# Performance work log

Measured on AMD Instinct MI355X. Metric: run time of the kernel, lower is better.

The kernel has to match this reference:

```python
import jax, jax.numpy as jnp
import numpy as np

N, E, D, H1, H2 = 50000, 800000, 128, 128, 128


def setup_inputs() -> dict:
    key = jax.random.key(0)
    ks = jax.random.split(key, 9)
    s = 0.05
    return {
        "x": jax.random.normal(ks[0], (N, D), dtype=jnp.float32),
        "edge_index": jax.random.randint(ks[1], (2, E), 0, N, dtype=jnp.int64),
        "W_l1": jax.random.normal(ks[2], (D, H1), dtype=jnp.float32) * s,
        "b_l1": jnp.zeros((H1,), dtype=jnp.float32),
        "W_r1": jax.random.normal(ks[3], (D, H1), dtype=jnp.float32) * s,
        "W_l2": jax.random.normal(ks[4], (H1, H2), dtype=jnp.float32) * s,
        "b_l2": jnp.zeros((H2,), dtype=jnp.float32),
        "W_r2": jax.random.normal(ks[5], (H1, H2), dtype=jnp.float32) * s,
        "W_e": jax.random.normal(ks[6], (2 * H2, 1), dtype=jnp.float32) * s,
        "b_e": jnp.zeros((1,), dtype=jnp.float32),
    }


def _sage_conv(h, src, tgt, n_nodes, W_l, b_l, W_r):
    # PyG SAGEConv (mean aggr): out = lin_l(mean_{j in N(i)} h_j) + lin_r(h_i)
    msg = h[src]                                              # [E, F] gather
    agg = jax.ops.segment_sum(msg, tgt, num_segments=n_nodes)  # [N, F]
    cnt = jax.ops.segment_sum(jnp.ones((src.shape[0], 1), h.dtype), tgt,
                              num_segments=n_nodes)            # [N, 1]
    mean = agg / jnp.maximum(cnt, 1.0)                         # empty nbrs -> 0
    return mean @ W_l + b_l + h @ W_r


def reference(x, edge_index, W_l1, b_l1, W_r1, W_l2, b_l2, W_r2, W_e, b_e):
    src, tgt = edge_index[0], edge_index[1]
    n_nodes = x.shape[0]
    h = jax.nn.relu(_sage_conv(x, src, tgt, n_nodes, W_l1, b_l1, W_r1))
    # dropout is identity in eval mode
    h = _sage_conv(h, src, tgt, n_nodes, W_l2, b_l2, W_r2)
    z = jnp.concatenate([h[src], h[tgt]], axis=-1)  # [E, 2*H2]
    y = z @ W_e + b_e                                # [E, 1]
    return jax.nn.sigmoid(y)
```

## Files before the change

kernel.cpp:

```cpp
#include <hip/hip_runtime.h>

#define NN 50000
#define NE 800000
#define DD 128
#define BUCKETS 196
#define PB 4096
#define PBLK 196
#define EMAX 6144
#define BPAD 264
#define PACKB 3125
#define WTB 128

typedef unsigned int uint_t;
typedef unsigned short ush_t;
typedef __attribute__((ext_vector_type(8))) short short8;
typedef __attribute__((ext_vector_type(4))) float f32x4;

__device__ __forceinline__ float bflo(uint_t u) { return __uint_as_float(u << 16); }
__device__ __forceinline__ float bfhi(uint_t u) { return __uint_as_float(u & 0xffff0000u); }
__device__ __forceinline__ ush_t f2bf(float f) {
  uint_t u = __float_as_uint(f);
  u += 0x7fffu + ((u >> 16) & 1u);
  return (ush_t)(u >> 16);
}
__device__ __forceinline__ uint_t pack2(float a, float b) {
  return (uint_t)f2bf(a) | ((uint_t)f2bf(b) << 16);
}

__device__ __forceinline__ int ld_idx(const void* ei, int is64, long long i) {
  return is64 ? (int)((const long long*)ei)[i] : ((const int*)ei)[i];
}

__device__ __forceinline__ int detect64(const void* ei) {
  const unsigned long long* p = (const unsigned long long*)ei;
  unsigned long long w = p[threadIdx.x & 63];
  return __ballot((w >> 32) != 0) == 0ull ? 1 : 0;
}

__device__ __forceinline__ int block_incl_scan(int v, int tid, int* wsum) {
  int lane = tid & 63, wave = tid >> 6;
  int s = v;
#pragma unroll
  for (int off = 1; off < 64; off <<= 1) {
    int u = __shfl_up(s, off, 64);
    if (lane >= off) s += u;
  }
  if (lane == 63) wsum[wave] = s;
  __syncthreads();
  int base = 0;
  if (wave > 0) base += wsum[0];
  if (wave > 1) base += wsum[1];
  if (wave > 2) base += wsum[2];
  return base + s;
}

__global__ __launch_bounds__(256) void prep_part_k(
    const void* __restrict__ ei, int* __restrict__ bcur,
    uint_t* __restrict__ pbuf, uint_t* __restrict__ epk,
    const float* __restrict__ x, ush_t* __restrict__ xbc,
    const float* __restrict__ Wl1, const float* __restrict__ Wr1,
    const float* __restrict__ Wl2, const float* __restrict__ Wr2,
    const float* __restrict__ We, const float* __restrict__ bl2,
    const float* __restrict__ be,
    ush_t* __restrict__ Wt1, float* __restrict__ uv, float* __restrict__ cc) {
  __shared__ int hist[256];
  __shared__ int basel[256];
  __shared__ int cur[256];
  __shared__ int gbase[256];
  __shared__ int wsum[4];
  __shared__ uint_t buf[PB];
  __shared__ unsigned char bbuf[PB];
  int tid = threadIdx.x;
  int blk = blockIdx.x;
  if (blk >= PBLK) {
    int blk2 = blk - PBLK;
    if (blk2 < 2) {
      const float* W = blk2 ? Wr2 : Wl2;
      int base = blk2 * 256;
      int wave = tid >> 6, lane = tid & 63;
      float e0 = We[lane], e1 = We[64 + lane];
      float f0 = We[128 + lane], f1 = We[192 + lane];
      for (int k = wave * 32; k < wave * 32 + 32; ++k) {
        float m0 = W[k * DD + lane];
        float m1 = W[k * DD + 64 + lane];
        float p = m0 * e0 + m1 * e1;
        float q = m0 * f0 + m1 * f1;
#pragma unroll
        for (int off = 32; off > 0; off >>= 1) {
          p += __shfl_down(p, off, 64);
          q += __shfl_down(q, off, 64);
        }
        if (lane == 0) {
          uv[base + k] = p;
          uv[base + 128 + k] = q;
        }
      }
      return;
    }
    if (blk2 == 2) {
      if (tid < 64) {
        int k = tid;
        float p = bl2[k] * (We[k] + We[128 + k]) +
                  bl2[k + 64] * (We[k + 64] + We[192 + k]);
#pragma unroll
        for (int off = 32; off > 0; off >>= 1) p += __shfl_down(p, off, 64);
        if (k == 0) cc[0] = p + be[0];
      }
      return;
    }
    blk2 -= 3;
    if (blk2 < PACKB) {
      int i = blk2 * 256 + tid;
      int node = i >> 4;
      int g = i & 15;
      const float4* xp = reinterpret_cast<const float4*>(x) + (size_t)i * 2;
      float4 v0 = xp[0];
      float4 v1 = xp[1];
      uint4 o;
      o.x = pack2(v0.x, v0.y);
      o.y = pack2(v0.z, v0.w);
      o.z = pack2(v1.x, v1.y);
      o.w = pack2(v1.z, v1.w);
      int chunk = g >> 2;
      int off32 = (g & 3) * 8;
      *reinterpret_cast<uint4*>(xbc + ((size_t)chunk * NN + node) * 32 + off32) = o;
      return;
    }
    blk2 -= PACKB;
    int e = blk2 * 256 + tid;
    int col = e >> 8;
    int k = e & 255;
    float v = (k < DD) ? Wl1[k * DD + col] : Wr1[(k - DD) * DD + col];
    Wt1[col * 256 + k] = f2bf(v);
    return;
  }
  int is64 = detect64(ei);
  hist[tid] = 0;
  __syncthreads();
  long long base = (long long)blk * PB;
  uint_t pv[PB / 256];
#pragma unroll
  for (int i = 0; i < PB / 256; ++i) {
    long long e = base + i * 256 + tid;
    if (e < NE) {
      int s = ld_idx(ei, is64, e);
      int d = ld_idx(ei, is64, (long long)NE + e);
      pv[i] = ((uint_t)(d >> 8) << 24) | ((uint_t)(d & 255) << 16) | (uint_t)s;
      epk[e] = ((uint_t)d << 16) | (uint_t)s;
      atomicAdd(&hist[d >> 8], 1);
    } else {
      pv[i] = 0xFFFFFFFFu;
    }
  }
  __syncthreads();
  int hv = hist[tid];
  int incl = block_incl_scan(hv, tid, wsum);
  basel[tid] = incl - hv;
  cur[tid] = incl - hv;
  if (hv > 0) gbase[tid] = atomicAdd(&bcur[tid], hv);
  __syncthreads();
#pragma unroll
  for (int i = 0; i < PB / 256; ++i) {
    uint_t p = pv[i];
    if (p != 0xFFFFFFFFu) {
      int b = p >> 24;
      int r = atomicAdd(&cur[b], 1);
      buf[r] = p & 0xFFFFFFu;
      bbuf[r] = (unsigned char)b;
    }
  }
  __syncthreads();
  int total = basel[255] + hist[255];
  for (int j = tid; j < total; j += 256) {
    int b = bbuf[j];
    int slot = gbase[b] + (j - basel[b]);
    if (slot < EMAX) pbuf[(size_t)b * EMAX + slot] = buf[j];
  }
}

__global__ __launch_bounds__(256) void csr_k(const uint_t* __restrict__ pbuf,
                                             const int* __restrict__ bcur,
                                             int* __restrict__ offsets,
                                             ush_t* __restrict__ srclist) {
  __shared__ int cnt[256];
  __shared__ int scur[256];
  __shared__ int wsum[4];
  __shared__ int sgb, scnt, stot;
  __shared__ uint_t ebuf[EMAX];
  int tid = threadIdx.x;
  int b = blockIdx.x;
  int v = 0;
  if (tid < BUCKETS) {
    v = bcur[tid];
    if (v > EMAX) v = EMAX;
  }
  int incl = block_incl_scan(v, tid, wsum);
  if (tid == b) { sgb = incl - v; scnt = v; }
  if (tid == BUCKETS - 1) stot = incl;
  cnt[tid] = 0;
  __syncthreads();
  int gb = sgb;
  int ecnt = scnt;
  for (int j = tid; j < ecnt; j += 256) {
    uint_t e = pbuf[(size_t)b * EMAX + j];
    ebuf[j] = e;
    atomicAdd(&cnt[(e >> 16) & 255], 1);
  }
  __syncthreads();
  int c = cnt[tid];
  int incl2 = block_incl_scan(c, tid, wsum);
  int ex = incl2 - c;
  scur[tid] = ex;
  int node = b * 256 + tid;
  if (node < NN) offsets[node] = gb + ex;
  if (b == BUCKETS - 1 && tid == 0) offsets[NN] = stot;
  __syncthreads();
  for (int j = tid; j < ecnt; j += 256) {
    uint_t e = ebuf[j];
    int p = atomicAdd(&scur[(e >> 16) & 255], 1);
    srclist[gb + p] = (ush_t)(e & 0xFFFFu);
  }
}

__global__ __launch_bounds__(256) void agg_k(const ush_t* __restrict__ xbc,
                                             const ush_t* __restrict__ srclist,
                                             const int* __restrict__ offsets,
                                             ush_t* __restrict__ meanb) {
  int bid = blockIdx.x;
  int chunk = bid & 3;
  int grp = bid >> 2;
  int tid = threadIdx.x;
  int node = grp * 64 + (tid >> 2);
  if (node >= NN) return;
  int l4 = tid & 3;
  int lane = tid & 63;
  int lb = lane & 60;
  const ush_t* base = xbc + (size_t)chunk * NN * 32 + l4 * 8;
  int beg = offsets[node];
  int end = offsets[node + 1];
  float a0 = 0.f, a1 = 0.f, a2 = 0.f, a3 = 0.f;
  float a4 = 0.f, a5 = 0.f, a6 = 0.f, a7 = 0.f;
  for (int c = beg; c < end; c += 16) {
    int m = end - c;
    int i0 = c + l4, i1 = c + 4 + l4, i2 = c + 8 + l4, i3 = c + 12 + l4;
    int s0 = (i0 < end) ? (int)srclist[i0] : 0;
    int s1 = (i1 < end) ? (int)srclist[i1] : 0;
    int s2 = (i2 < end) ? (int)srclist[i2] : 0;
    int s3 = (i3 < end) ? (int)srclist[i3] : 0;
    uint4 v[16];
#pragma unroll
    for (int j = 0; j < 4; ++j)
      v[j] = *reinterpret_cast<const uint4*>(base + (size_t)__shfl(s0, lb + j, 64) * 32);
#pragma unroll
    for (int j = 0; j < 4; ++j)
      v[4 + j] = *reinterpret_cast<const uint4*>(base + (size_t)__shfl(s1, lb + j, 64) * 32);
#pragma unroll
    for (int j = 0; j < 4; ++j)
      v[8 + j] = *reinterpret_cast<const uint4*>(base + (size_t)__shfl(s2, lb + j, 64) * 32);
#pragma unroll
    for (int j = 0; j < 4; ++j)
      v[12 + j] = *reinterpret_cast<const uint4*>(base + (size_t)__shfl(s3, lb + j, 64) * 32);
#pragma unroll
    for (int j = 0; j < 16; ++j) {
      if (j < m) {
        a0 += bflo(v[j].x); a1 += bfhi(v[j].x);
        a2 += bflo(v[j].y); a3 += bfhi(v[j].y);
        a4 += bflo(v[j].z); a5 += bfhi(v[j].z);
        a6 += bflo(v[j].w); a7 += bfhi(v[j].w);
      }
    }
  }
  float inv = 1.0f / fmaxf((float)(end - beg), 1.0f);
  uint4 o;
  o.x = pack2(a0 * inv, a1 * inv);
  o.y = pack2(a2 * inv, a3 * inv);
  o.z = pack2(a4 * inv, a5 * inv);
  o.w = pack2(a6 * inv, a7 * inv);
  *reinterpret_cast<uint4*>(meanb + (size_t)node * DD + chunk * 32 + l4 * 8) = o;
}

__global__ __launch_bounds__(256, 2) void sage_l1(
    const ush_t* __restrict__ meanb, const ush_t* __restrict__ xbc,
    const ush_t* __restrict__ Wt1, const float* __restrict__ bl,
    const float* __restrict__ uv, float2* __restrict__ t12,
    float2* __restrict__ r12) {
  __shared__ ush_t sB[128 * BPAD];
  int tid = threadIdx.x;
  int lane = tid & 63;
  int wave = tid >> 6;
  int n15 = lane & 15, quad = lane >> 4;
  int nb = blockIdx.x * 64;
#pragma unroll
  for (int it = 0; it < 16; ++it) {
    int i = it * 256 + tid;
    int col = i >> 5, c = i & 31;
    *reinterpret_cast<short8*>(&sB[col * BPAD + c * 8]) =
        reinterpret_cast<const short8*>(Wt1)[i];
  }
  __syncthreads();
  int row = nb + wave * 16 + n15;
  int arow = (row < NN) ? row : (NN - 1);
  const ush_t* a0 = meanb + (size_t)arow * DD;
  f32x4 acc[8];
#pragma unroll
  for (int t = 0; t < 8; ++t) acc[t] = (f32x4){0.f, 0.f, 0.f, 0.f};
#pragma unroll
  for (int c = 0; c < 8; ++c) {
    short8 af;
    if (c < 4) {
      af = *reinterpret_cast<const short8*>(a0 + c * 32 + quad * 8);
    } else {
      af = *reinterpret_cast<const short8*>(
          xbc + ((size_t)(c - 4) * NN + arow) * 32 + quad * 8);
    }
    int kb = c * 32 + quad * 8;
#pragma unroll
    for (int t = 0; t < 8; ++t) {
      short8 bf = *reinterpret_cast<const short8*>(&sB[(t * 16 + n15) * BPAD + kb]);
      acc[t] = __builtin_amdgcn_mfma_f32_16x16x32_bf16(af, bf, acc[t], 0, 0, 0);
    }
  }
  float p1[4] = {0.f, 0.f, 0.f, 0.f};
  float p2[4] = {0.f, 0.f, 0.f, 0.f};
  float q1[4] = {0.f, 0.f, 0.f, 0.f};
  float q2[4] = {0.f, 0.f, 0.f, 0.f};
#pragma unroll
  for (int t = 0; t < 8; ++t) {
    int col = t * 16 + n15;
    float b = bl[col];
    float U1 = uv[col];
    float U2 = uv[128 + col];
    float V1 = uv[256 + col];
    float V2 = uv[384 + col];
#pragma unroll
    for (int reg = 0; reg < 4; ++reg) {
      float h = fmaxf(acc[t][reg] + b, 0.f);
      p1[reg] += h * U1;
      p2[reg] += h * U2;
      q1[reg] += h * V1;
      q2[reg] += h * V2;
    }
  }
#pragma unroll
  for (int reg = 0; reg < 4; ++reg) {
    float a1 = p1[reg], a2 = p2[reg], b1 = q1[reg], b2 = q2[reg];
    for (int off = 8; off > 0; off >>= 1) {
      a1 += __shfl_down(a1, off, 16);
      a2 += __shfl_down(a2, off, 16);
      b1 += __shfl_down(b1, off, 16);
      b2 += __shfl_down(b2, off, 16);
    }
    int r = nb + wave * 16 + quad * 4 + reg;
    if (n15 == 0 && r < NN) {
      t12[r] = make_float2(a1, a2);
      r12[r] = make_float2(b1, b2);
    }
  }
}

__global__ __launch_bounds__(256) void agg2s_k(const float2* __restrict__ t12,
                                               const ush_t* __restrict__ srclist,
                                               const int* __restrict__ offsets,
                                               const float2* __restrict__ r12,
                                               float2* __restrict__ s12) {
  int t = blockIdx.x * 256 + threadIdx.x;
  int node = t >> 4;
  int lane = t & 15;
  int beg = offsets[node];
  int end = offsets[node + 1];
  float sx = 0.f, sy = 0.f;
  for (int c = beg + lane; c < end; c += 16) {
    int s = srclist[c];
    float2 v = t12[s];
    sx += v.x;
    sy += v.y;
  }
  for (int off = 8; off > 0; off >>= 1) {
    sx += __shfl_down(sx, off, 16);
    sy += __shfl_down(sy, off, 16);
  }
  if (lane == 0) {
    float inv = 1.0f / fmaxf((float)(end - beg), 1.0f);
    float2 r = r12[node];
    s12[node] = make_float2(sx * inv + r.x, sy * inv + r.y);
  }
}

__global__ __launch_bounds__(256) void edge_k(const uint_t* __restrict__ epk,
                                              const float2* __restrict__ s12,
                                              const float* __restrict__ cc,
                                              float* __restrict__ out) {
  int e = blockIdx.x * 256 + threadIdx.x;
  uint_t p = epk[e];
  float2 a = s12[p & 0xFFFFu];
  float2 b = s12[p >> 16];
  float v = a.x + b.y + cc[0];
  out[e] = 1.0f / (1.0f + __expf(-v));
}

extern "C" void kernel_launch(void* const* d_in, const int* in_sizes, int n_in,
                              void* d_out, int out_size, void* d_ws, size_t ws_size,
                              hipStream_t stream) {
  const float* x   = (const float*)d_in[0];
  const void*  ei  = d_in[1];
  const float* Wl1 = (const float*)d_in[2];
  const float* bl1 = (const float*)d_in[3];
  const float* Wr1 = (const float*)d_in[4];
  const float* Wl2 = (const float*)d_in[5];
  const float* bl2 = (const float*)d_in[6];
  const float* Wr2 = (const float*)d_in[7];
  const float* We  = (const float*)d_in[8];
  const float* be  = (const float*)d_in[9];
  float* out = (float*)d_out;

  int* bcur       = (int*)d_ws;
  int* offsets    = bcur + 256;
  uint_t* epk     = (uint_t*)(offsets + 50004);
  uint_t* pbuf    = epk + NE;
  ush_t* srclist  = (ush_t*)(pbuf + (size_t)BUCKETS * EMAX);
  ush_t* xbc      = srclist + NE;
  ush_t* meanb    = xbc + (size_t)NN * DD;
  float2* t12     = (float2*)(meanb + (size_t)NN * DD);
  float2* r12     = t12 + NN;
  float2* s12     = r12 + NN;
  ush_t* Wt1      = (ush_t*)(s12 + NN);
  float* uv       = (float*)(Wt1 + 32768);
  float* cc       = uv + 512;

  hipMemsetAsync(bcur, 0, 256 * sizeof(int), stream);
  prep_part_k<<<PBLK + 3 + PACKB + WTB, 256, 0, stream>>>(
      ei, bcur, pbuf, epk, x, xbc, Wl1, Wr1, Wl2, Wr2, We, bl2, be, Wt1, uv, cc);
  csr_k<<<BUCKETS, 256, 0, stream>>>(pbuf, bcur, offsets, srclist);

  agg_k<<<((NN + 63) / 64) * 4, 256, 0, stream>>>(xbc, srclist, offsets, meanb);

  sage_l1<<<(NN + 63) / 64, 256, 0, stream>>>(meanb, xbc, Wt1, bl1, uv, t12, r12);

  agg2s_k<<<(NN * 16) / 256, 256, 0, stream>>>(t12, srclist, offsets, r12, s12);

  edge_k<<<NE / 256, 256, 0, stream>>>(epk, s12, cc, out);
}
```

Before: 182.4 us.

## Move x packing into CSR kernel and use 16-feature chunks for aggregation

Moves the x-to-bf16 packing, weight transpose and uv precompute blocks out of the partition kernel and into the CSR kernel launch, so they overlap with CSR building instead of partitioning. Changes the packed-x layout from 4 chunks of 32 features to 8 chunks of 16, so agg_k launches twice as many blocks that each gather 8-byte rows, and adds nontemporal stores. The aim is more parallelism in the gather and better load balance across kernels. In exchange, each gather fetches fewer bytes, which raises the number of index shuffles and load instructions per feature.

```diff
diff --git a/kernel.cpp b/kernel.cpp
--- a/kernel.cpp
+++ b/kernel.cpp
@@ -12,6 +12,7 @@
 #define WTB 128
 
 typedef unsigned int uint_t;
+typedef unsigned long long ull_t;
 typedef unsigned short ush_t;
 typedef __attribute__((ext_vector_type(8))) short short8;
 typedef __attribute__((ext_vector_type(4))) float f32x4;
@@ -56,13 +57,7 @@
 
 __global__ __launch_bounds__(256) void prep_part_k(
     const void* __restrict__ ei, int* __restrict__ bcur,
-    uint_t* __restrict__ pbuf, uint_t* __restrict__ epk,
-    const float* __restrict__ x, ush_t* __restrict__ xbc,
-    const float* __restrict__ Wl1, const float* __restrict__ Wr1,
-    const float* __restrict__ Wl2, const float* __restrict__ Wr2,
-    const float* __restrict__ We, const float* __restrict__ bl2,
-    const float* __restrict__ be,
-    ush_t* __restrict__ Wt1, float* __restrict__ uv, float* __restrict__ cc) {
+    uint_t* __restrict__ pbuf, uint_t* __restrict__ epk) {
   __shared__ int hist[256];
   __shared__ int basel[256];
   __shared__ int cur[256];
@@ -72,8 +67,68 @@
   __shared__ unsigned char bbuf[PB];
   int tid = threadIdx.x;
   int blk = blockIdx.x;
-  if (blk >= PBLK) {
-    int blk2 = blk - PBLK;
+  int is64 = detect64(ei);
+  hist[tid] = 0;
+  __syncthreads();
+  long long base = (long long)blk * PB;
+  uint_t pv[PB / 256];
+#pragma unroll
+  for (int i = 0; i < PB / 256; ++i) {
+    long long e = base + i * 256 + tid;
+    if (e < NE) {
+      int s = ld_idx(ei, is64, e);
+      int d = ld_idx(ei, is64, (long long)NE + e);
+      pv[i] = ((uint_t)(d >> 8) << 24) | ((uint_t)(d & 255) << 16) | (uint_t)s;
+      epk[e] = ((uint_t)d << 16) | (uint_t)s;
+      atomicAdd(&hist[d >> 8], 1);
+    } else {
+      pv[i] = 0xFFFFFFFFu;
+    }
+  }
+  __syncthreads();
+  int hv = hist[tid];
+  int incl = block_incl_scan(hv, tid, wsum);
+  basel[tid] = incl - hv;
+  cur[tid] = incl - hv;
+  if (hv > 0) gbase[tid] = atomicAdd(&bcur[tid], hv);
+  __syncthreads();
+#pragma unroll
+  for (int i = 0; i < PB / 256; ++i) {
+    uint_t p = pv[i];
+    if (p != 0xFFFFFFFFu) {
+      int b = p >> 24;
+      int r = atomicAdd(&cur[b], 1);
+      buf[r] = p & 0xFFFFFFu;
+      bbuf[r] = (unsigned char)b;
+    }
+  }
+  __syncthreads();
+  int total = basel[255] + hist[255];
+  for (int j = tid; j < total; j += 256) {
+    int b = bbuf[j];
+    int slot = gbase[b] + (j - basel[b]);
+    if (slot < EMAX) pbuf[(size_t)b * EMAX + slot] = buf[j];
+  }
+}
+
+__global__ __launch_bounds__(256) void csr_k(
+    const uint_t* __restrict__ pbuf, const int* __restrict__ bcur,
+    int* __restrict__ offsets, ush_t* __restrict__ srclist,
+    const float* __restrict__ x, ush_t* __restrict__ xbc,
+    const float* __restrict__ Wl1, const float* __restrict__ Wr1,
+    const float* __restrict__ Wl2, const float* __restrict__ Wr2,
+    const float* __restrict__ We, const float* __restrict__ bl2,
+    const float* __restrict__ be,
+    ush_t* __restrict__ Wt1, float* __restrict__ uv, float* __restrict__ cc) {
+  __shared__ int cnt[256];
+  __shared__ int scur[256];
+  __shared__ int wsum[4];
+  __shared__ int sgb, scnt, stot;
+  __shared__ uint_t ebuf[EMAX];
+  int tid = threadIdx.x;
+  int b = blockIdx.x;
+  if (b >= BUCKETS) {
+    int blk2 = b - BUCKETS;
     if (blk2 < 2) {
       const float* W = blk2 ? Wr2 : Wl2;
       int base = blk2 * 256;
@@ -116,14 +171,16 @@
       const float4* xp = reinterpret_cast<const float4*>(x) + (size_t)i * 2;
       float4 v0 = xp[0];
       float4 v1 = xp[1];
-      uint4 o;
-      o.x = pack2(v0.x, v0.y);
-      o.y = pack2(v0.z, v0.w);
-      o.z = pack2(v1.x, v1.y);
-      o.w = pack2(v1.z, v1.w);
-      int chunk = g >> 2;
-      int off32 = (g & 3) * 8;
-      *reinterpret_cast<uint4*>(xbc + ((size_t)chunk * NN + node) * 32 + off32) = o;
+      uint_t oa = pack2(v0.x, v0.y);
+      uint_t ob = pack2(v0.z, v0.w);
+      uint_t oc = pack2(v1.x, v1.y);
+      uint_t od = pack2(v1.z, v1.w);
+      int chunk = g >> 1;
+      int off16 = (g & 1) * 8;
+      ull_t* dst = reinterpret_cast<ull_t*>(
+          xbc + ((size_t)chunk * NN + node) * 16 + off16);
+      __builtin_nontemporal_store(((ull_t)ob << 32) | oa, dst);
+      __builtin_nontemporal_store(((ull_t)od << 32) | oc, dst + 1);
       return;
     }
     blk2 -= PACKB;
@@ -134,61 +191,6 @@
     Wt1[col * 256 + k] = f2bf(v);
     return;
   }
-  int is64 = detect64(ei);
-  hist[tid] = 0;
-  __syncthreads();
-  long long base = (long long)blk * PB;
-  uint_t pv[PB / 256];
-#pragma unroll
-  for (int i = 0; i < PB / 256; ++i) {
-    long long e = base + i * 256 + tid;
-    if (e < NE) {
-      int s = ld_idx(ei, is64, e);
-      int d = ld_idx(ei, is64, (long long)NE + e);
-      pv[i] = ((uint_t)(d >> 8) << 24) | ((uint_t)(d & 255) << 16) | (uint_t)s;
-      epk[e] = ((uint_t)d << 16) | (uint_t)s;
-      atomicAdd(&hist[d >> 8], 1);
-    } else {
-      pv[i] = 0xFFFFFFFFu;
-    }
-  }
-  __syncthreads();
-  int hv = hist[tid];
-  int incl = block_incl_scan(hv, tid, wsum);
-  basel[tid] = incl - hv;
-  cur[tid] = incl - hv;
-  if (hv > 0) gbase[tid] = atomicAdd(&bcur[tid], hv);
-  __syncthreads();
-#pragma unroll
-  for (int i = 0; i < PB / 256; ++i) {
-    uint_t p = pv[i];
-    if (p != 0xFFFFFFFFu) {
-      int b = p >> 24;
-      int r = atomicAdd(&cur[b], 1);
-      buf[r] = p & 0xFFFFFFu;
-      bbuf[r] = (unsigned char)b;
-    }
-  }
-  __syncthreads();
-  int total = basel[255] + hist[255];
-  for (int j = tid; j < total; j += 256) {
-    int b = bbuf[j];
-    int slot = gbase[b] + (j - basel[b]);
-    if (slot < EMAX) pbuf[(size_t)b * EMAX + slot] = buf[j];
-  }
-}
-
-__global__ __launch_bounds__(256) void csr_k(const uint_t* __restrict__ pbuf,
-                                             const int* __restrict__ bcur,
-                                             int* __restrict__ offsets,
-                                             ush_t* __restrict__ srclist) {
-  __shared__ int cnt[256];
-  __shared__ int scur[256];
-  __shared__ int wsum[4];
-  __shared__ int sgb, scnt, stot;
-  __shared__ uint_t ebuf[EMAX];
-  int tid = threadIdx.x;
-  int b = blockIdx.x;
   int v = 0;
   if (tid < BUCKETS) {
     v = bcur[tid];
@@ -227,19 +229,18 @@
                                              const int* __restrict__ offsets,
                                              ush_t* __restrict__ meanb) {
   int bid = blockIdx.x;
-  int chunk = bid & 3;
-  int grp = bid >> 2;
+  int chunk = bid & 7;
+  int grp = bid >> 3;
   int tid = threadIdx.x;
   int node = grp * 64 + (tid >> 2);
   if (node >= NN) return;
   int l4 = tid & 3;
   int lane = tid & 63;
   int lb = lane & 60;
-  const ush_t* base = xbc + (size_t)chunk * NN * 32 + l4 * 8;
+  const ush_t* base = xbc + (size_t)chunk * NN * 16 + l4 * 4;
   int beg = offsets[node];
   int end = offsets[node + 1];
   float a0 = 0.f, a1 = 0.f, a2 = 0.f, a3 = 0.f;
-  float a4 = 0.f, a5 = 0.f, a6 = 0.f, a7 = 0.f;
   for (int c = beg; c < end; c += 16) {
     int m = end - c;
     int i0 = c + l4, i1 = c + 4 + l4, i2 = c + 8 + l4, i3 = c + 12 + l4;
@@ -247,36 +248,33 @@
     int s1 = (i1 < end) ? (int)srclist[i1] : 0;
     int s2 = (i2 < end) ? (int)srclist[i2] : 0;
     int s3 = (i3 < end) ? (int)srclist[i3] : 0;
-    uint4 v[16];
+    uint2 v[16];
 #pragma unroll
     for (int j = 0; j < 4; ++j)
-      v[j] = *reinterpret_cast<const uint4*>(base + (size_t)__shfl(s0, lb + j, 64) * 32);
+      v[j] = *reinterpret_cast<const uint2*>(base + (size_t)__shfl(s0, lb + j, 64) * 16);
 #pragma unroll
     for (int j = 0; j < 4; ++j)
-      v[4 + j] = *reinterpret_cast<const uint4*>(base + (size_t)__shfl(s1, lb + j, 64) * 32);
+      v[4 + j] = *reinterpret_cast<const uint2*>(base + (size_t)__shfl(s1, lb + j, 64) * 16);
 #pragma unroll
     for (int j = 0; j < 4; ++j)
-      v[8 + j] = *reinterpret_cast<const uint4*>(base + (size_t)__shfl(s2, lb + j, 64) * 32);
+      v[8 + j] = *reinterpret_cast<const uint2*>(base + (size_t)__shfl(s2, lb + j, 64) * 16);
 #pragma unroll
     for (int j = 0; j < 4; ++j)
-      v[12 + j] = *reinterpret_cast<const uint4*>(base + (size_t)__shfl(s3, lb + j, 64) * 32);
+      v[12 + j] = *reinterpret_cast<const uint2*>(base + (size_t)__shfl(s3, lb + j, 64) * 16);
 #pragma unroll
     for (int j = 0; j < 16; ++j) {
       if (j < m) {
         a0 += bflo(v[j].x); a1 += bfhi(v[j].x);
         a2 += bflo(v[j].y); a3 += bfhi(v[j].y);
-        a4 += bflo(v[j].z); a5 += bfhi(v[j].z);
-        a6 += bflo(v[j].w); a7 += bfhi(v[j].w);
       }
     }
   }
   float inv = 1.0f / fmaxf((float)(end - beg), 1.0f);
-  uint4 o;
-  o.x = pack2(a0 * inv, a1 * inv);
-  o.y = pack2(a2 * inv, a3 * inv);
-  o.z = pack2(a4 * inv, a5 * inv);
-  o.w = pack2(a6 * inv, a7 * inv);
-  *reinterpret_cast<uint4*>(meanb + (size_t)node * DD + chunk * 32 + l4 * 8) = o;
+  uint_t o0 = pack2(a0 * inv, a1 * inv);
+  uint_t o1 = pack2(a2 * inv, a3 * inv);
+  __builtin_nontemporal_store(
+      ((ull_t)o1 << 32) | o0,
+      reinterpret_cast<ull_t*>(meanb + (size_t)node * DD + chunk * 16 + l4 * 4));
 }
 
 __global__ __launch_bounds__(256, 2) void sage_l1(
@@ -310,8 +308,9 @@
     if (c < 4) {
       af = *reinterpret_cast<const short8*>(a0 + c * 32 + quad * 8);
     } else {
+      int fb = (c - 4) * 32 + quad * 8;
       af = *reinterpret_cast<const short8*>(
-          xbc + ((size_t)(c - 4) * NN + arow) * 32 + quad * 8);
+          xbc + ((size_t)(fb >> 4) * NN + arow) * 16 + (fb & 15));
     }
     int kb = c * 32 + quad * 8;
 #pragma unroll
@@ -428,11 +427,13 @@
   float* cc       = uv + 512;
 
   hipMemsetAsync(bcur, 0, 256 * sizeof(int), stream);
-  prep_part_k<<<PBLK + 3 + PACKB + WTB, 256, 0, stream>>>(
-      ei, bcur, pbuf, epk, x, xbc, Wl1, Wr1, Wl2, Wr2, We, bl2, be, Wt1, uv, cc);
-  csr_k<<<BUCKETS, 256, 0, stream>>>(pbuf, bcur, offsets, srclist);
-
-  agg_k<<<((NN + 63) / 64) * 4, 256, 0, stream>>>(xbc, srclist, offsets, meanb);
+  prep_part_k<<<PBLK, 256, 0, stream>>>(ei, bcur, pbuf, epk);
+
+  csr_k<<<BUCKETS + 3 + PACKB + WTB, 256, 0, stream>>>(
+      pbuf, bcur, offsets, srclist, x, xbc, Wl1, Wr1, Wl2, Wr2, We, bl2, be,
+      Wt1, uv, cc);
+
+  agg_k<<<((NN + 63) / 64) * 8, 256, 0, stream>>>(xbc, srclist, offsets, meanb);
 
   sage_l1<<<(NN + 63) / 64, 256, 0, stream>>>(meanb, xbc, Wt1, bl1, uv, t12, r12);
 
```

Result: slower. 195.0 us (+6.9%).
